# Kernel optimization log

Hardware: AMD Instinct MI355X
Metric: run time of the kernel (lower is better)

## Reference

```python
import jax, jax.numpy as jnp
import numpy as np

N_SENT = 131072
NUM_BAGS = 8192
REL_DIM = 690
NUM_CLASSES = 53


def setup_inputs() -> dict:
    key = jax.random.key(0)
    k1, k2, k3, k4, k5, k6 = jax.random.split(key, 6)
    x = jax.random.normal(k1, (N_SENT, REL_DIM), dtype=jnp.float32)
    relation_weight = jax.random.normal(k2, (NUM_CLASSES, REL_DIM), dtype=jnp.float32) * 0.06
    attention_weight = jax.random.normal(k3, (NUM_CLASSES, REL_DIM), dtype=jnp.float32) * 0.06
    bias = jax.random.normal(k4, (NUM_CLASSES,), dtype=jnp.float32)
    attention_query = jax.random.randint(k5, (N_SENT,), 0, NUM_CLASSES, dtype=jnp.int32)
    # strictly increasing bag boundaries: 0 < b_1 < ... < b_{B-1} < N
    interior = jax.random.choice(k6, N_SENT - 1, shape=(NUM_BAGS - 1,), replace=False) + 1
    scope = jnp.concatenate([jnp.zeros((1,), jnp.int32),
                             jnp.sort(interior).astype(jnp.int32),
                             jnp.full((1,), N_SENT, jnp.int32)])
    return {"x": x, "relation_weight": relation_weight,
            "attention_weight": attention_weight, "bias": bias,
            "attention_query": attention_query, "scope": scope}


def reference(x, relation_weight, attention_weight, bias, attention_query, scope):
    N = x.shape[0]
    B = scope.shape[0] - 1  # num bags
    # map each sentence to its bag: scope[b] <= i < scope[b+1]
    seg = jnp.searchsorted(scope[1:], jnp.arange(N), side="right")

    # per-sentence attention logit: sum(x * att_emb * rel_emb) over feature dim
    rel_q = relation_weight[attention_query]   # [N, D]
    att_q = attention_weight[attention_query]  # [N, D]
    logit = jnp.sum(x * att_q * rel_q, axis=1)  # [N]

    # segment softmax over each bag (numerically stable)
    seg_max = jax.ops.segment_max(logit, seg, num_segments=B)  # [B]
    e = jnp.exp(logit - seg_max[seg])                           # [N]
    denom = jax.ops.segment_sum(e, seg, num_segments=B)        # [B]
    w = e / denom[seg]                                          # [N]

    # attention-weighted bag representation
    bag_repre = jax.ops.segment_sum(w[:, None] * x, seg, num_segments=B)  # [B, D]

    # dropout with drop_prob = 0.0 -> identity
    logits = bag_repre @ relation_weight.T + bias  # [B, C]
    return logits
```

## Files before the change

kernel.cpp:

```cpp
#include <hip/hip_runtime.h>
#include <math.h>

#define NSENT 131072
#define NBAGS 8192
#define DIM   690
#define NCLS  53
#define PAIRS 345

__global__ void comb_kernel(const float* __restrict__ att,
                            const float* __restrict__ rel,
                            float* __restrict__ comb) {
    int i = blockIdx.x * 256 + threadIdx.x;
    if (i < NCLS * DIM) comb[i] = att[i] * rel[i];
}

template <bool USE_COMB>
__global__ __launch_bounds__(256) void bag_attn_kernel(
        const float* __restrict__ x,
        const float* __restrict__ rel,
        const float* __restrict__ att,
        const float* __restrict__ bias,
        const int*   __restrict__ query,
        const int*   __restrict__ scope,
        const float* __restrict__ comb,
        float*       __restrict__ out) {
    const int b     = blockIdx.x;
    const int tid   = threadIdx.x;
    const int wave  = tid >> 6;
    const int lane  = tid & 63;

    const int start = scope[b];
    const int end   = scope[b + 1];

    float2 acc[6];
#pragma unroll
    for (int k = 0; k < 6; ++k) acc[k] = make_float2(0.f, 0.f);
    float m = -INFINITY;
    float l = 0.f;

    for (int i = start + wave; i < end; i += 4) {
        const float2* xrow = (const float2*)(x + (size_t)i * DIM);
        const int q = query[i];

        float2 xv[6];
        float partial = 0.f;
        if (USE_COMB) {
            const float2* crow = (const float2*)(comb + (size_t)q * DIM);
#pragma unroll
            for (int k = 0; k < 6; ++k) {
                const int p = lane + 64 * k;
                if (p < PAIRS) {
                    xv[k] = xrow[p];
                    const float2 cv = crow[p];
                    partial += xv[k].x * cv.x + xv[k].y * cv.y;
                } else {
                    xv[k] = make_float2(0.f, 0.f);
                }
            }
        } else {
            const float2* rrow = (const float2*)(rel + (size_t)q * DIM);
            const float2* arow = (const float2*)(att + (size_t)q * DIM);
#pragma unroll
            for (int k = 0; k < 6; ++k) {
                const int p = lane + 64 * k;
                if (p < PAIRS) {
                    xv[k] = xrow[p];
                    const float2 rv = rrow[p];
                    const float2 av = arow[p];
                    partial += xv[k].x * rv.x * av.x + xv[k].y * rv.y * av.y;
                } else {
                    xv[k] = make_float2(0.f, 0.f);
                }
            }
        }

#pragma unroll
        for (int off = 32; off >= 1; off >>= 1)
            partial += __shfl_xor(partial, off, 64);
        const float logit = partial;

        const float mn    = fmaxf(m, logit);
        const float scale = expf(m - mn);
        const float e     = expf(logit - mn);
        l = l * scale + e;
#pragma unroll
        for (int k = 0; k < 6; ++k) {
            acc[k].x = acc[k].x * scale + e * xv[k].x;
            acc[k].y = acc[k].y * scale + e * xv[k].y;
        }
        m = mn;
    }

    __shared__ float s_m[4];
    __shared__ float s_l[4];
    __shared__ float s_acc[4][DIM];
    __shared__ float s_rep[DIM];

    if (lane == 0) { s_m[wave] = m; s_l[wave] = l; }
    __syncthreads();

    const float M = fmaxf(fmaxf(s_m[0], s_m[1]), fmaxf(s_m[2], s_m[3]));
    const float factor = (l > 0.f) ? expf(m - M) : 0.f;
#pragma unroll
    for (int k = 0; k < 6; ++k) {
        const int p = lane + 64 * k;
        if (p < PAIRS) {
            s_acc[wave][2 * p]     = acc[k].x * factor;
            s_acc[wave][2 * p + 1] = acc[k].y * factor;
        }
    }
    __syncthreads();

    float Ltot = 0.f;
#pragma unroll
    for (int w = 0; w < 4; ++w) {
        const float fw = (s_l[w] > 0.f) ? expf(s_m[w] - M) : 0.f;
        Ltot += s_l[w] * fw;
    }
    const float inv = 1.f / Ltot;

    for (int d = tid; d < DIM; d += 256) {
        s_rep[d] = (s_acc[0][d] + s_acc[1][d] + s_acc[2][d] + s_acc[3][d]) * inv;
    }
    __syncthreads();

    for (int c = wave; c < NCLS; c += 4) {
        const float2* rrow = (const float2*)(rel + (size_t)c * DIM);
        float partial = 0.f;
#pragma unroll
        for (int k = 0; k < 6; ++k) {
            const int p = lane + 64 * k;
            if (p < PAIRS) {
                const float2 rv = rrow[p];
                partial += rv.x * s_rep[2 * p] + rv.y * s_rep[2 * p + 1];
            }
        }
#pragma unroll
        for (int off = 32; off >= 1; off >>= 1)
            partial += __shfl_xor(partial, off, 64);
        if (lane == 0) out[(size_t)b * NCLS + c] = partial + bias[c];
    }
}

extern "C" void kernel_launch(void* const* d_in, const int* in_sizes, int n_in,
                              void* d_out, int out_size, void* d_ws, size_t ws_size,
                              hipStream_t stream) {
    const float* x     = (const float*)d_in[0];
    const float* rel   = (const float*)d_in[1];
    const float* att   = (const float*)d_in[2];
    const float* bias  = (const float*)d_in[3];
    const int*   query = (const int*)d_in[4];
    const int*   scope = (const int*)d_in[5];
    float*       out   = (float*)d_out;

    const size_t comb_bytes = (size_t)NCLS * DIM * sizeof(float);
    if (ws_size >= comb_bytes) {
        float* comb = (float*)d_ws;
        comb_kernel<<<(NCLS * DIM + 255) / 256, 256, 0, stream>>>(att, rel, comb);
        bag_attn_kernel<true><<<NBAGS, 256, 0, stream>>>(
            x, rel, att, bias, query, scope, comb, out);
    } else {
        bag_attn_kernel<false><<<NBAGS, 256, 0, stream>>>(
            x, rel, att, bias, query, scope, nullptr, out);
    }
}
```

Baseline: 597.9 us.

## Split bag attention into one-wave-per-bag streaming kernel and separate output GEMM

Each bag is now handled by a single wave instead of a 256-thread block. The wave software-prefetches the next sentence row while it reduces the current one, so no cross-wave LDS merge or barriers are needed. The bag representations go to a workspace buffer, and a separate tiled kernel computes the final 53-class projection with the relation weights staged in shared memory. This removes per-bag block overhead and the redundant per-block reload of relation weights. In exchange it adds an extra global write and read of the bag representations, an extra launch, and serial latency inside each wave. Fast exp intrinsics also replace expf.

Measured after the change: 798.7 us. 1.34x slower.

```diff
diff --git a/kernel.cpp b/kernel.cpp
--- a/kernel.cpp
+++ b/kernel.cpp
@@ -14,93 +14,202 @@
     if (i < NCLS * DIM) comb[i] = att[i] * rel[i];
 }
 
-template <bool USE_COMB>
-__global__ __launch_bounds__(256) void bag_attn_kernel(
+__global__ __launch_bounds__(256, 8) void bag_stream_kernel(
+        const float* __restrict__ x,
+        const float* __restrict__ comb,
+        const int*   __restrict__ query,
+        const int*   __restrict__ scope,
+        float*       __restrict__ repre) {
+    const int bag  = blockIdx.x * 4 + (threadIdx.x >> 6);
+    const int lane = threadIdx.x & 63;
+    const int start = scope[bag];
+    const int end   = scope[bag + 1];
+
+    float2 acc[6];
+#pragma unroll
+    for (int k = 0; k < 6; ++k) acc[k] = make_float2(0.f, 0.f);
+    float m = -INFINITY;
+    float l = 0.f;
+
+    int q = query[start];
+    float2 xv[6];
+    {
+        const float2* xrow = (const float2*)(x + (size_t)start * DIM);
+#pragma unroll
+        for (int k = 0; k < 6; ++k) {
+            const int p = lane + 64 * k;
+            xv[k] = (p < PAIRS) ? xrow[p] : make_float2(0.f, 0.f);
+        }
+    }
+
+    for (int i = start; i < end; ++i) {
+        const float2* crow = (const float2*)(comb + (size_t)q * DIM);
+        float partial = 0.f;
+#pragma unroll
+        for (int k = 0; k < 6; ++k) {
+            const int p = lane + 64 * k;
+            if (p < PAIRS) {
+                const float2 cv = crow[p];
+                partial += xv[k].x * cv.x + xv[k].y * cv.y;
+            }
+        }
+
+        float2 xn[6];
+        int qn = 0;
+        const bool more = (i + 1 < end);
+        if (more) {
+            qn = query[i + 1];
+            const float2* xrow = (const float2*)(x + (size_t)(i + 1) * DIM);
+#pragma unroll
+            for (int k = 0; k < 6; ++k) {
+                const int p = lane + 64 * k;
+                xn[k] = (p < PAIRS) ? xrow[p] : make_float2(0.f, 0.f);
+            }
+        } else {
+#pragma unroll
+            for (int k = 0; k < 6; ++k) xn[k] = make_float2(0.f, 0.f);
+        }
+
+#pragma unroll
+        for (int off = 32; off >= 1; off >>= 1)
+            partial += __shfl_xor(partial, off, 64);
+
+        const float mn = fmaxf(m, partial);
+        const float sc = __expf(m - mn);
+        const float e  = __expf(partial - mn);
+        l = l * sc + e;
+#pragma unroll
+        for (int k = 0; k < 6; ++k) {
+            acc[k].x = acc[k].x * sc + e * xv[k].x;
+            acc[k].y = acc[k].y * sc + e * xv[k].y;
+        }
+        m = mn;
+
+#pragma unroll
+        for (int k = 0; k < 6; ++k) xv[k] = xn[k];
+        q = qn;
+    }
+
+    const float inv = 1.f / l;
+    float2* rrow = (float2*)(repre + (size_t)bag * DIM);
+#pragma unroll
+    for (int k = 0; k < 6; ++k) {
+        const int p = lane + 64 * k;
+        if (p < PAIRS)
+            rrow[p] = make_float2(acc[k].x * inv, acc[k].y * inv);
+    }
+}
+
+#define K3_BPB 32
+#define K3_CD  230
+
+__global__ __launch_bounds__(256) void out_gemm_kernel(
+        const float* __restrict__ repre,
+        const float* __restrict__ rel,
+        const float* __restrict__ bias,
+        float*       __restrict__ out) {
+    __shared__ float s_rel[NCLS * K3_CD];
+
+    const int t     = threadIdx.x;
+    const int co    = t & 7;
+    const int bag_l = t >> 3;
+    const int bag   = blockIdx.x * K3_BPB + bag_l;
+
+    float acc[7];
+#pragma unroll
+    for (int k = 0; k < 7; ++k) acc[k] = 0.f;
+
+    for (int chunk = 0; chunk < 3; ++chunk) {
+        const int d0 = chunk * K3_CD;
+        for (int idx = t; idx < NCLS * K3_CD; idx += 256) {
+            const int row = idx / K3_CD;
+            const int col = idx - row * K3_CD;
+            s_rel[idx] = rel[(size_t)row * DIM + d0 + col];
+        }
+        __syncthreads();
+
+        const float2* rep2 = (const float2*)(repre + (size_t)bag * DIM + d0);
+        const float2* srl2 = (const float2*)s_rel;
+        for (int d2 = 0; d2 < K3_CD / 2; ++d2) {
+            const float2 xd = rep2[d2];
+#pragma unroll
+            for (int k = 0; k < 7; ++k) {
+                const int c = co + 8 * k;
+                if (c < NCLS) {
+                    const float2 rv = srl2[c * (K3_CD / 2) + d2];
+                    acc[k] += xd.x * rv.x + xd.y * rv.y;
+                }
+            }
+        }
+        __syncthreads();
+    }
+
+#pragma unroll
+    for (int k = 0; k < 7; ++k) {
+        const int c = co + 8 * k;
+        if (c < NCLS) out[(size_t)bag * NCLS + c] = acc[k] + bias[c];
+    }
+}
+
+__global__ __launch_bounds__(256) void bag_attn_fallback(
         const float* __restrict__ x,
         const float* __restrict__ rel,
         const float* __restrict__ att,
         const float* __restrict__ bias,
         const int*   __restrict__ query,
         const int*   __restrict__ scope,
-        const float* __restrict__ comb,
         float*       __restrict__ out) {
-    const int b     = blockIdx.x;
-    const int tid   = threadIdx.x;
-    const int wave  = tid >> 6;
-    const int lane  = tid & 63;
-
+    const int b    = blockIdx.x;
+    const int tid  = threadIdx.x;
+    const int wave = tid >> 6;
+    const int lane = tid & 63;
     const int start = scope[b];
     const int end   = scope[b + 1];
 
     float2 acc[6];
 #pragma unroll
     for (int k = 0; k < 6; ++k) acc[k] = make_float2(0.f, 0.f);
-    float m = -INFINITY;
-    float l = 0.f;
+    float m = -INFINITY, l = 0.f;
 
     for (int i = start + wave; i < end; i += 4) {
         const float2* xrow = (const float2*)(x + (size_t)i * DIM);
         const int q = query[i];
-
+        const float2* rrow = (const float2*)(rel + (size_t)q * DIM);
+        const float2* arow = (const float2*)(att + (size_t)q * DIM);
         float2 xv[6];
         float partial = 0.f;
-        if (USE_COMB) {
-            const float2* crow = (const float2*)(comb + (size_t)q * DIM);
-#pragma unroll
-            for (int k = 0; k < 6; ++k) {
-                const int p = lane + 64 * k;
-                if (p < PAIRS) {
-                    xv[k] = xrow[p];
-                    const float2 cv = crow[p];
-                    partial += xv[k].x * cv.x + xv[k].y * cv.y;
-                } else {
-                    xv[k] = make_float2(0.f, 0.f);
-                }
-            }
-        } else {
-            const float2* rrow = (const float2*)(rel + (size_t)q * DIM);
-            const float2* arow = (const float2*)(att + (size_t)q * DIM);
-#pragma unroll
-            for (int k = 0; k < 6; ++k) {
-                const int p = lane + 64 * k;
-                if (p < PAIRS) {
-                    xv[k] = xrow[p];
-                    const float2 rv = rrow[p];
-                    const float2 av = arow[p];
-                    partial += xv[k].x * rv.x * av.x + xv[k].y * rv.y * av.y;
-                } else {
-                    xv[k] = make_float2(0.f, 0.f);
-                }
-            }
-        }
-
+#pragma unroll
+        for (int k = 0; k < 6; ++k) {
+            const int p = lane + 64 * k;
+            if (p < PAIRS) {
+                xv[k] = xrow[p];
+                const float2 rv = rrow[p];
+                const float2 av = arow[p];
+                partial += xv[k].x * rv.x * av.x + xv[k].y * rv.y * av.y;
+            } else xv[k] = make_float2(0.f, 0.f);
+        }
 #pragma unroll
         for (int off = 32; off >= 1; off >>= 1)
             partial += __shfl_xor(partial, off, 64);
-        const float logit = partial;
-
-        const float mn    = fmaxf(m, logit);
-        const float scale = expf(m - mn);
-        const float e     = expf(logit - mn);
-        l = l * scale + e;
-#pragma unroll
-        for (int k = 0; k < 6; ++k) {
-            acc[k].x = acc[k].x * scale + e * xv[k].x;
-            acc[k].y = acc[k].y * scale + e * xv[k].y;
+        const float mn = fmaxf(m, partial);
+        const float sc = __expf(m - mn);
+        const float e  = __expf(partial - mn);
+        l = l * sc + e;
+#pragma unroll
+        for (int k = 0; k < 6; ++k) {
+            acc[k].x = acc[k].x * sc + e * xv[k].x;
+            acc[k].y = acc[k].y * sc + e * xv[k].y;
         }
         m = mn;
     }
 
-    __shared__ float s_m[4];
-    __shared__ float s_l[4];
+    __shared__ float s_m[4], s_l[4];
     __shared__ float s_acc[4][DIM];
     __shared__ float s_rep[DIM];
-
     if (lane == 0) { s_m[wave] = m; s_l[wave] = l; }
     __syncthreads();
-
     const float M = fmaxf(fmaxf(s_m[0], s_m[1]), fmaxf(s_m[2], s_m[3]));
-    const float factor = (l > 0.f) ? expf(m - M) : 0.f;
+    const float factor = (l > 0.f) ? __expf(m - M) : 0.f;
 #pragma unroll
     for (int k = 0; k < 6; ++k) {
         const int p = lane + 64 * k;
@@ -110,30 +219,24 @@
         }
     }
     __syncthreads();
-
     float Ltot = 0.f;
 #pragma unroll
     for (int w = 0; w < 4; ++w) {
-        const float fw = (s_l[w] > 0.f) ? expf(s_m[w] - M) : 0.f;
+        const float fw = (s_l[w] > 0.f) ? __expf(s_m[w] - M) : 0.f;
         Ltot += s_l[w] * fw;
     }
     const float inv = 1.f / Ltot;
-
-    for (int d = tid; d < DIM; d += 256) {
+    for (int d = tid; d < DIM; d += 256)
         s_rep[d] = (s_acc[0][d] + s_acc[1][d] + s_acc[2][d] + s_acc[3][d]) * inv;
-    }
     __syncthreads();
-
     for (int c = wave; c < NCLS; c += 4) {
         const float2* rrow = (const float2*)(rel + (size_t)c * DIM);
         float partial = 0.f;
 #pragma unroll
         for (int k = 0; k < 6; ++k) {
             const int p = lane + 64 * k;
-            if (p < PAIRS) {
-                const float2 rv = rrow[p];
-                partial += rv.x * s_rep[2 * p] + rv.y * s_rep[2 * p + 1];
-            }
+            if (p < PAIRS)
+                partial += rrow[p].x * s_rep[2 * p] + rrow[p].y * s_rep[2 * p + 1];
         }
 #pragma unroll
         for (int off = 32; off >= 1; off >>= 1)
@@ -153,14 +256,17 @@
     const int*   scope = (const int*)d_in[5];
     float*       out   = (float*)d_out;
 
-    const size_t comb_bytes = (size_t)NCLS * DIM * sizeof(float);
-    if (ws_size >= comb_bytes) {
-        float* comb = (float*)d_ws;
+    const size_t comb_bytes  = (size_t)NCLS * DIM * sizeof(float);
+    const size_t comb_pad    = (comb_bytes + 255) & ~(size_t)255;
+    const size_t repre_bytes = (size_t)NBAGS * DIM * sizeof(float);
+
+    if (ws_size >= comb_pad + repre_bytes) {
+        float* comb  = (float*)d_ws;
+        float* repre = (float*)((char*)d_ws + comb_pad);
         comb_kernel<<<(NCLS * DIM + 255) / 256, 256, 0, stream>>>(att, rel, comb);
-        bag_attn_kernel<true><<<NBAGS, 256, 0, stream>>>(
-            x, rel, att, bias, query, scope, comb, out);
+        bag_stream_kernel<<<NBAGS / 4, 256, 0, stream>>>(x, comb, query, scope, repre);
+        out_gemm_kernel<<<NBAGS / K3_BPB, 256, 0, stream>>>(repre, rel, bias, out);
     } else {
-        bag_attn_kernel<false><<<NBAGS, 256, 0, stream>>>(
-            x, rel, att, bias, query, scope, nullptr, out);
-    }
-}
+        bag_attn_fallback<<<NBAGS, 256, 0, stream>>>(x, rel, att, bias, query, scope, out);
+    }
+}
```
